# Kernel optimization log

Measured on AMD Instinct MI355X. Metric: run time of the kernel, lower is better.

## Reference

```python
import jax, jax.numpy as jnp
import numpy as np
import math

B, H, L, DK = 4, 16, 4096, 64
LK0 = 4096
LOG_LK = int(math.log(LK0))  # 8
LOG_L = int(math.log(L))     # 8
NC = 3
D_MODEL = H * DK             # 1024


def setup_inputs() -> dict:
    key = jax.random.key(0)
    ks = jax.random.split(key, 20)
    s = 0.02  # small init scale for stability of softmax/clustering
    f = jnp.float32
    return dict(
        Q=jax.random.normal(ks[0], (B, H, L, DK), f),
        K=jax.random.normal(ks[1], (B, H, LK0, DK), f),
        V=jax.random.normal(ks[2], (B, H, LK0, DK), f),
        shrink_k_w=jax.random.normal(ks[3], (LOG_LK, LK0), f) * s,
        shrink_k_b=jax.random.normal(ks[4], (LOG_LK,), f) * s,
        shrink_v_w=jax.random.normal(ks[5], (LOG_LK, LK0), f) * s,
        shrink_v_b=jax.random.normal(ks[6], (LOG_LK,), f) * s,
        shrink_q_w=jax.random.normal(ks[7], (LOG_L, L), f) * s,
        shrink_q_b=jax.random.normal(ks[8], (LOG_L,), f) * s,
        pk_w=jax.random.normal(ks[9], (NC, LOG_LK * D_MODEL), f) * s,
        pk_b=jax.random.normal(ks[10], (NC,), f) * s,
        pq_w=jax.random.normal(ks[11], (NC, LOG_L * D_MODEL), f) * s,
        pq_b=jax.random.normal(ks[12], (NC,), f) * s,
        qp_w=jax.random.normal(ks[13], (NC, NC), f) * s,
        qp_b=jax.random.normal(ks[14], (NC,), f) * s,
        kp_w=jax.random.normal(ks[15], (NC, NC), f) * s,
        kp_b=jax.random.normal(ks[16], (NC,), f) * s,
    )


def reference(Q, K, V, shrink_k_w, shrink_k_b, shrink_v_w, shrink_v_b,
              shrink_q_w, shrink_q_b, pk_w, pk_b, pq_w, pq_b,
              qp_w, qp_b, kp_w, kp_b):
    b, h, l, d_k = Q.shape
    # shrink along sequence axis (Linear over seq after permute in torch)
    Ks = jnp.einsum('bhkd,mk->bhmd', K, shrink_k_w) + shrink_k_b[None, None, :, None]
    Vs = jnp.einsum('bhkd,mk->bhmd', V, shrink_v_w) + shrink_v_b[None, None, :, None]
    Qs = jnp.einsum('bhqd,mq->bhmd', Q, shrink_q_w) + shrink_q_b[None, None, :, None]
    lk = Ks.shape[2]  # = LOG_LK
    # cluster logits -> soft assignments
    ckp = jax.nn.relu(Ks.reshape(b, -1) @ pk_w.T + pk_b)
    cqp = jax.nn.relu(Qs.reshape(b, -1) @ pq_w.T + pq_b)
    cluster_q = jax.nn.softmax(cqp @ qp_w.T + qp_b, axis=-1)
    cluster_k = jax.nn.softmax(ckp @ kp_w.T + kp_b, axis=-1)
    mu = jnp.mean(cluster_q, axis=0)
    sigma = jax.nn.softplus(jnp.std(cluster_k, axis=0, ddof=1))  # torch.std is unbiased
    logp = -0.5 * jnp.square((cluster_k - mu) / sigma) - jnp.log(sigma) - 0.5 * jnp.log(2.0 * jnp.pi)
    # CrossEntropyLoss with soft targets: -mean_b sum_c target*log_softmax(input)
    ce = jnp.mean(-jnp.sum(cluster_q * jax.nn.log_softmax(cluster_q, axis=-1), axis=-1))
    loss = -jnp.mean(logp) + ce

    inds_q = jnp.argmax(cluster_q, axis=-1)  # [b]
    inds_k = jnp.argmax(cluster_k, axis=-1)  # [b]
    # get_group masks whole batches whose cluster == i+1 (per-batch constant mask;
    # the reshape round-trip in the original is an identity on [b,h,seq,d])
    mask_tril = jnp.tril(jnp.ones((l, lk), dtype=bool))  # True positions get -1e9
    nc = qp_b.shape[0]
    scores_center = jnp.zeros((nc, b, h, l, lk), Q.dtype)
    row_idx = jnp.broadcast_to(inds_q[:, None, None], (b, h, l))  # q_ind[:,:,:,0]
    bi = jnp.arange(b)[:, None, None]
    hi = jnp.arange(h)[None, :, None]
    scale = 1.0 / jnp.sqrt(jnp.asarray(d_k, Q.dtype))
    for i in range(nc):
        gQ = jnp.where((inds_q != i + 1)[:, None, None, None], Q, 0.0)
        gK = jnp.where((inds_k != i + 1)[:, None, None, None], Ks, 0.0)
        s = jnp.einsum('bhqd,bhkd->bhqk', gQ, gK) * scale  # [b,h,l,lk]
        s = jnp.where(mask_tril, -1e9, s)
        # original repeats gK lk times along a c-axis, softmaxes, then means over c:
        # all c-copies are identical, so mean over c == the per-copy value; then [0]
        sm0 = jax.nn.softmax(s, axis=-1)[0]  # [h,l,lk] (batch 0, as in original)
        scores_center = scores_center.at[i, bi, hi, row_idx, :].set(
            jnp.broadcast_to(sm0, (b, h, l, lk)))
    final_score = jnp.max(scores_center, axis=0)  # [b,h,l,lk]
    attn = jax.nn.softmax(final_score, axis=-1)
    context = jnp.einsum('bhqk,bhkd->bhqd', attn, Vs)
    return context, loss
```

## Files before the change

kernel.cpp:

```cpp
#include <hip/hip_runtime.h>
#include <hip/hip_bf16.h>
#include <math.h>

#define BB   4
#define HH   16
#define LL   4096
#define DKK  64
#define MM   8
#define NCC  3
#define BH   (BB*HH)
#define ROWS_PER_CHUNK 512
#define NCHUNK (LL/ROWS_PER_CHUNK)
#define CTX_ELEMS (BB*HH*LL*DKK)

#define DOTS_OFF 98304

__global__ __launch_bounds__(256) void shrink_kernel(
    const float* __restrict__ Q, const float* __restrict__ K,
    const float* __restrict__ V,
    const float* __restrict__ skw, const float* __restrict__ svw,
    const float* __restrict__ sqw,
    float* __restrict__ ws)
{
    __shared__ float lds[12288];

    int bx    = blockIdx.x;
    int input = bx >> 9;
    int rem   = bx & 511;
    int bh    = rem >> 3;
    int chunk = rem & 7;

    const float* X; const float* W;
    if (input == 0)      { X = K; W = skw; }
    else if (input == 1) { X = V; W = svw; }
    else                 { X = Q; W = sqw; }

    int t  = threadIdx.x;
    int k0 = chunk * ROWS_PER_CHUNK;

    #pragma unroll
    for (int m = 0; m < MM; ++m)
        for (int k = t; k < ROWS_PER_CHUNK; k += 256)
            lds[k*8 + m] = W[m*LL + k0 + k];
    __syncthreads();

    int d4     = (t & 15) * 4;
    int stripe = t >> 4;

    const float* base = X + (size_t)bh * LL * DKK;

    float4 acc[MM];
    #pragma unroll
    for (int m = 0; m < MM; ++m) acc[m] = make_float4(0.f, 0.f, 0.f, 0.f);

    for (int i = 0; i < ROWS_PER_CHUNK/16; ++i) {
        int kp = i*16 + stripe;
        float4 v = *reinterpret_cast<const float4*>(
            base + (size_t)(k0 + kp) * DKK + d4);
        float4 w0 = *reinterpret_cast<const float4*>(&lds[kp*8]);
        float4 w1 = *reinterpret_cast<const float4*>(&lds[kp*8 + 4]);
        float wm[MM] = {w0.x, w0.y, w0.z, w0.w, w1.x, w1.y, w1.z, w1.w};
        #pragma unroll
        for (int m = 0; m < MM; ++m) {
            float w = wm[m];
            acc[m].x = fmaf(v.x, w, acc[m].x);
            acc[m].y = fmaf(v.y, w, acc[m].y);
            acc[m].z = fmaf(v.z, w, acc[m].z);
            acc[m].w = fmaf(v.w, w, acc[m].w);
        }
    }
    __syncthreads();

    float* red = lds + 4096;
    #pragma unroll
    for (int m = 0; m < MM; ++m) {
        red[t*32 + m*4 + 0] = acc[m].x;
        red[t*32 + m*4 + 1] = acc[m].y;
        red[t*32 + m*4 + 2] = acc[m].z;
        red[t*32 + m*4 + 3] = acc[m].w;
    }
    __syncthreads();

    float* wsb = ws + ((size_t)input * BH + bh) * 512;
    for (int out = t; out < 512; out += 256) {
        int m  = out >> 6;
        int d  = out & 63;
        int dg = d >> 2, dj = d & 3;
        float s = 0.f;
        #pragma unroll
        for (int st = 0; st < 16; ++st)
            s += red[(st*16 + dg)*32 + m*4 + dj];
        atomicAdd(wsb + out, s);
    }
}

__global__ __launch_bounds__(256) void dot_kernel(
    const float* __restrict__ ws,
    const float* __restrict__ skb, const float* __restrict__ sqb,
    const float* __restrict__ pk_w, const float* __restrict__ pk_b,
    const float* __restrict__ pq_w, const float* __restrict__ pq_b,
    float* __restrict__ dots)
{
    __shared__ float red[4];
    int idx = blockIdx.x;
    int isQ = idx >= 12;
    int g   = idx - (isQ ? 12 : 0);
    int b   = g / NCC;
    int c   = g % NCC;

    const float* xs   = ws + (size_t)(isQ ? 2 : 0) * (BH * 512) + (size_t)b * 8192;
    const float* pw   = (isQ ? pq_w : pk_w) + (size_t)c * 8192;
    const float* bias = isQ ? sqb : skb;

    float bl[MM];
    #pragma unroll
    for (int m = 0; m < MM; ++m) bl[m] = bias[m];

    int t = threadIdx.x;
    float acc = 0.f;
    #pragma unroll
    for (int i = 0; i < 8; ++i) {
        int e = i*256 + t;
        int m = (e >> 4) & 7;
        float4 x = *reinterpret_cast<const float4*>(xs + (size_t)e * 4);
        float4 w = *reinterpret_cast<const float4*>(pw + (size_t)e * 4);
        float bm = bl[m];
        acc = fmaf(x.x + bm, w.x, acc);
        acc = fmaf(x.y + bm, w.y, acc);
        acc = fmaf(x.z + bm, w.z, acc);
        acc = fmaf(x.w + bm, w.w, acc);
    }
    #pragma unroll
    for (int off = 1; off < 64; off <<= 1) acc += __shfl_xor(acc, off);
    int wave = t >> 6, lane = t & 63;
    if (lane == 0) red[wave] = acc;
    __syncthreads();
    if (t == 0) {
        float total = red[0] + red[1] + red[2] + red[3];
        float pb = (isQ ? pq_b : pk_b)[c];
        float r  = total + pb;
        dots[idx] = r > 0.f ? r : 0.f;
    }
}

__global__ __launch_bounds__(64) void final_kernel(
    const float* __restrict__ dots,
    const float* __restrict__ qp_w, const float* __restrict__ qp_b,
    const float* __restrict__ kp_w, const float* __restrict__ kp_b,
    float* __restrict__ out_loss)
{
    __shared__ float s_dots[24];
    __shared__ float s_qpw[9], s_qpb[3], s_kpw[9], s_kpb[3];
    int t = threadIdx.x;
    if (t < 24) s_dots[t] = dots[t];
    if (t < 9)  { s_qpw[t] = qp_w[t]; s_kpw[t] = kp_w[t]; }
    if (t < 3)  { s_qpb[t] = qp_b[t]; s_kpb[t] = kp_b[t]; }
    __syncthreads();

    if (t == 0) {
        float cq[BB][NCC], ck[BB][NCC];
        for (int b = 0; b < BB; ++b) {
            float lq[NCC], lk[NCC];
            for (int c = 0; c < NCC; ++c) {
                float sq = s_qpb[c], sk = s_kpb[c];
                for (int c2 = 0; c2 < NCC; ++c2) {
                    sq = fmaf(s_dots[12 + b*NCC + c2], s_qpw[c*NCC + c2], sq);
                    sk = fmaf(s_dots[b*NCC + c2],      s_kpw[c*NCC + c2], sk);
                }
                lq[c] = sq; lk[c] = sk;
            }
            float mq = fmaxf(fmaxf(lq[0], lq[1]), lq[2]);
            float mk = fmaxf(fmaxf(lk[0], lk[1]), lk[2]);
            float zq = 0.f, zk = 0.f;
            for (int c = 0; c < NCC; ++c) {
                cq[b][c] = expf(lq[c] - mq); zq += cq[b][c];
                ck[b][c] = expf(lk[c] - mk); zk += ck[b][c];
            }
            for (int c = 0; c < NCC; ++c) { cq[b][c] /= zq; ck[b][c] /= zk; }
        }
        float mu[NCC], mk_[NCC], sigma[NCC];
        for (int c = 0; c < NCC; ++c) {
            float s1 = 0.f, s2 = 0.f;
            for (int b = 0; b < BB; ++b) { s1 += cq[b][c]; s2 += ck[b][c]; }
            mu[c]  = s1 * 0.25f;
            mk_[c] = s2 * 0.25f;
        }
        for (int c = 0; c < NCC; ++c) {
            float v = 0.f;
            for (int b = 0; b < BB; ++b) {
                float d = ck[b][c] - mk_[c];
                v = fmaf(d, d, v);
            }
            float stdv = sqrtf(v / (BB - 1));
            sigma[c] = log1pf(expf(stdv));
        }
        const float HALF_LOG_2PI = 0.9189385332046727f;
        float sum_logp = 0.f;
        for (int b = 0; b < BB; ++b)
            for (int c = 0; c < NCC; ++c) {
                float z = (ck[b][c] - mu[c]) / sigma[c];
                sum_logp += -0.5f*z*z - logf(sigma[c]) - HALF_LOG_2PI;
            }
        float ce = 0.f;
        for (int b = 0; b < BB; ++b) {
            float mx = fmaxf(fmaxf(cq[b][0], cq[b][1]), cq[b][2]);
            float z = 0.f;
            for (int c = 0; c < NCC; ++c) z += expf(cq[b][c] - mx);
            float lse = mx + logf(z);
            float s = 0.f;
            for (int c = 0; c < NCC; ++c) s += cq[b][c] * (cq[b][c] - lse);
            ce += -s;
        }
        ce *= 0.25f;
        float loss = -(sum_logp / (BB * NCC)) + ce;
        out_loss[0] = loss;
    }
}

__global__ __launch_bounds__(256) void broadcast_kernel(
    const float* __restrict__ ws, const float* __restrict__ svb,
    float* __restrict__ out)
{
    int bx = blockIdx.x;
    int bh = bx >> 4;
    int lc = bx & 15;
    int t  = threadIdx.x;
    int d4     = (t & 15) * 4;
    int stripe = t >> 4;

    const float* vs = ws + ((size_t)1 * BH + bh) * 512;
    float bias = 0.f;
    #pragma unroll
    for (int m = 0; m < MM; ++m) bias += svb[m];
    bias *= 0.125f;

    float4 c = make_float4(bias, bias, bias, bias);
    #pragma unroll
    for (int m = 0; m < MM; ++m) {
        c.x += 0.125f * vs[m*64 + d4 + 0];
        c.y += 0.125f * vs[m*64 + d4 + 1];
        c.z += 0.125f * vs[m*64 + d4 + 2];
        c.w += 0.125f * vs[m*64 + d4 + 3];
    }

    float* obase = out + (size_t)bh * LL * DKK + (size_t)lc * 256 * DKK;
    #pragma unroll
    for (int i = 0; i < 16; ++i) {
        int l = i*16 + stripe;
        *reinterpret_cast<float4*>(obase + (size_t)l * DKK + d4) = c;
    }
}

extern "C" void kernel_launch(void* const* d_in, const int* in_sizes, int n_in,
                              void* d_out, int out_size, void* d_ws, size_t ws_size,
                              hipStream_t stream) {
    const float* Q    = (const float*)d_in[0];
    const float* K    = (const float*)d_in[1];
    const float* V    = (const float*)d_in[2];
    const float* skw  = (const float*)d_in[3];
    const float* skb  = (const float*)d_in[4];
    const float* svw  = (const float*)d_in[5];
    const float* svb  = (const float*)d_in[6];
    const float* sqw  = (const float*)d_in[7];
    const float* sqb  = (const float*)d_in[8];
    const float* pk_w = (const float*)d_in[9];
    const float* pk_b = (const float*)d_in[10];
    const float* pq_w = (const float*)d_in[11];
    const float* pq_b = (const float*)d_in[12];
    const float* qp_w = (const float*)d_in[13];
    const float* qp_b = (const float*)d_in[14];
    const float* kp_w = (const float*)d_in[15];
    const float* kp_b = (const float*)d_in[16];

    float* out = (float*)d_out;
    float* ws  = (float*)d_ws;

    hipMemsetAsync(ws, 0, (size_t)3 * BH * 512 * sizeof(float), stream);

    shrink_kernel<<<dim3(3 * BH * NCHUNK), dim3(256), 0, stream>>>(
        Q, K, V, skw, svw, sqw, ws);

    dot_kernel<<<dim3(24), dim3(256), 0, stream>>>(
        ws, skb, sqb, pk_w, pk_b, pq_w, pq_b, ws + DOTS_OFF);

    final_kernel<<<dim3(1), dim3(64), 0, stream>>>(
        ws + DOTS_OFF, qp_w, qp_b, kp_w, kp_b, out + (size_t)CTX_ELEMS);

    broadcast_kernel<<<dim3(BH * 16), dim3(256), 0, stream>>>(ws, svb, out);
}
```

Baseline: 276.8 us.

## Write per-chunk shrink partials without atomics and reduce them in consumers

The shrink kernel now uses 4 chunks of 1024 rows instead of 8 chunks of 512. It stores weights in m-major LDS, unrolls four row loads per iteration, and reduces across stripes with wave shuffles before a small padded LDS reduction. Each chunk writes its own partial slice, so the memset and global atomics go away, and the dot and broadcast kernels sum the four chunk partials when they read them. The cost is fewer blocks (768), which means less parallelism for the memory-bound streaming of Q, K and V, plus slightly more reads in the downstream kernels.

```diff
diff --git a/kernel.cpp b/kernel.cpp
--- a/kernel.cpp
+++ b/kernel.cpp
@@ -9,26 +9,27 @@
 #define MM   8
 #define NCC  3
 #define BH   (BB*HH)
-#define ROWS_PER_CHUNK 512
-#define NCHUNK (LL/ROWS_PER_CHUNK)
+#define NCHUNK 4
+#define ROWS_PER_CHUNK (LL/NCHUNK)
 #define CTX_ELEMS (BB*HH*LL*DKK)
 
-#define DOTS_OFF 98304
-
-__global__ __launch_bounds__(256) void shrink_kernel(
+#define DOTS_OFF (3*BH*NCHUNK*512)
+
+__global__ __launch_bounds__(256, 5) void shrink_kernel(
     const float* __restrict__ Q, const float* __restrict__ K,
     const float* __restrict__ V,
     const float* __restrict__ skw, const float* __restrict__ svw,
     const float* __restrict__ sqw,
     float* __restrict__ ws)
 {
-    __shared__ float lds[12288];
+    __shared__ float wlds[MM * ROWS_PER_CHUNK];
+    float* red = wlds;
 
     int bx    = blockIdx.x;
-    int input = bx >> 9;
-    int rem   = bx & 511;
-    int bh    = rem >> 3;
-    int chunk = rem & 7;
+    int input = bx >> 8;
+    int rem   = bx & 255;
+    int bh    = rem >> 2;
+    int chunk = rem & 3;
 
     const float* X; const float* W;
     if (input == 0)      { X = K; W = skw; }
@@ -40,57 +41,78 @@
 
     #pragma unroll
     for (int m = 0; m < MM; ++m)
-        for (int k = t; k < ROWS_PER_CHUNK; k += 256)
-            lds[k*8 + m] = W[m*LL + k0 + k];
-    __syncthreads();
-
-    int d4     = (t & 15) * 4;
+        #pragma unroll
+        for (int kk = 0; kk < ROWS_PER_CHUNK; kk += 256)
+            wlds[m*ROWS_PER_CHUNK + kk + t] = W[m*LL + k0 + kk + t];
+    __syncthreads();
+
+    int dg     = t & 15;
+    int d4     = dg * 4;
     int stripe = t >> 4;
 
-    const float* base = X + (size_t)bh * LL * DKK;
+    const float* base = X + (size_t)bh * LL * DKK + (size_t)k0 * DKK;
 
     float4 acc[MM];
     #pragma unroll
     for (int m = 0; m < MM; ++m) acc[m] = make_float4(0.f, 0.f, 0.f, 0.f);
 
-    for (int i = 0; i < ROWS_PER_CHUNK/16; ++i) {
-        int kp = i*16 + stripe;
-        float4 v = *reinterpret_cast<const float4*>(
-            base + (size_t)(k0 + kp) * DKK + d4);
-        float4 w0 = *reinterpret_cast<const float4*>(&lds[kp*8]);
-        float4 w1 = *reinterpret_cast<const float4*>(&lds[kp*8 + 4]);
-        float wm[MM] = {w0.x, w0.y, w0.z, w0.w, w1.x, w1.y, w1.z, w1.w};
+    for (int j = 0; j < ROWS_PER_CHUNK/64; ++j) {
+        float4 v[4];
+        #pragma unroll
+        for (int u = 0; u < 4; ++u) {
+            int row = j*64 + u*16 + stripe;
+            v[u] = *reinterpret_cast<const float4*>(base + (size_t)row * DKK + d4);
+        }
+        #pragma unroll
+        for (int u = 0; u < 4; ++u) {
+            int row = j*64 + u*16 + stripe;
+            #pragma unroll
+            for (int m = 0; m < MM; ++m) {
+                float w = wlds[m*ROWS_PER_CHUNK + row];
+                acc[m].x = fmaf(v[u].x, w, acc[m].x);
+                acc[m].y = fmaf(v[u].y, w, acc[m].y);
+                acc[m].z = fmaf(v[u].z, w, acc[m].z);
+                acc[m].w = fmaf(v[u].w, w, acc[m].w);
+            }
+        }
+    }
+
+    #pragma unroll
+    for (int m = 0; m < MM; ++m) {
+        acc[m].x += __shfl_xor(acc[m].x, 16);
+        acc[m].y += __shfl_xor(acc[m].y, 16);
+        acc[m].z += __shfl_xor(acc[m].z, 16);
+        acc[m].w += __shfl_xor(acc[m].w, 16);
+        acc[m].x += __shfl_xor(acc[m].x, 32);
+        acc[m].y += __shfl_xor(acc[m].y, 32);
+        acc[m].z += __shfl_xor(acc[m].z, 32);
+        acc[m].w += __shfl_xor(acc[m].w, 32);
+    }
+
+    __syncthreads();
+
+    int wave = t >> 6, lane = t & 63;
+    if (lane < 16) {
+        float* r = &red[(wave*16 + lane) * 33];
         #pragma unroll
         for (int m = 0; m < MM; ++m) {
-            float w = wm[m];
-            acc[m].x = fmaf(v.x, w, acc[m].x);
-            acc[m].y = fmaf(v.y, w, acc[m].y);
-            acc[m].z = fmaf(v.z, w, acc[m].z);
-            acc[m].w = fmaf(v.w, w, acc[m].w);
-        }
-    }
-    __syncthreads();
-
-    float* red = lds + 4096;
-    #pragma unroll
-    for (int m = 0; m < MM; ++m) {
-        red[t*32 + m*4 + 0] = acc[m].x;
-        red[t*32 + m*4 + 1] = acc[m].y;
-        red[t*32 + m*4 + 2] = acc[m].z;
-        red[t*32 + m*4 + 3] = acc[m].w;
-    }
-    __syncthreads();
-
-    float* wsb = ws + ((size_t)input * BH + bh) * 512;
-    for (int out = t; out < 512; out += 256) {
-        int m  = out >> 6;
-        int d  = out & 63;
-        int dg = d >> 2, dj = d & 3;
+            r[m*4 + 0] = acc[m].x;
+            r[m*4 + 1] = acc[m].y;
+            r[m*4 + 2] = acc[m].z;
+            r[m*4 + 3] = acc[m].w;
+        }
+    }
+    __syncthreads();
+
+    float* wsb = ws + (size_t)(((input*BH + bh)*NCHUNK + chunk)) * 512;
+    for (int o = t; o < 512; o += 256) {
+        int m = o >> 6, d = o & 63;
+        int dgg = d >> 2, dc = d & 3;
         float s = 0.f;
         #pragma unroll
-        for (int st = 0; st < 16; ++st)
-            s += red[(st*16 + dg)*32 + m*4 + dj];
-        atomicAdd(wsb + out, s);
+        for (int w = 0; w < 4; ++w)
+            s += red[(w*16 + dgg)*33 + m*4 + dc];
+        wsb[o] = s;
     }
 }
 
@@ -108,7 +130,7 @@
     int b   = g / NCC;
     int c   = g % NCC;
 
-    const float* xs   = ws + (size_t)(isQ ? 2 : 0) * (BH * 512) + (size_t)b * 8192;
+    int input = isQ ? 2 : 0;
     const float* pw   = (isQ ? pq_w : pk_w) + (size_t)c * 8192;
     const float* bias = isQ ? sqb : skb;
 
@@ -121,8 +143,16 @@
     #pragma unroll
     for (int i = 0; i < 8; ++i) {
         int e = i*256 + t;
+        int h = e >> 7;
         int m = (e >> 4) & 7;
-        float4 x = *reinterpret_cast<const float4*>(xs + (size_t)e * 4);
+        const float* xb = ws + (size_t)(((input*BH + b*HH + h)*NCHUNK)) * 512
+                             + (size_t)(e & 127) * 4;
+        float4 x = make_float4(0.f, 0.f, 0.f, 0.f);
+        #pragma unroll
+        for (int ch = 0; ch < NCHUNK; ++ch) {
+            float4 p = *reinterpret_cast<const float4*>(xb + ch*512);
+            x.x += p.x; x.y += p.y; x.z += p.z; x.w += p.w;
+        }
         float4 w = *reinterpret_cast<const float4*>(pw + (size_t)e * 4);
         float bm = bl[m];
         acc = fmaf(x.x + bm, w.x, acc);
@@ -228,7 +258,7 @@
     int d4     = (t & 15) * 4;
     int stripe = t >> 4;
 
-    const float* vs = ws + ((size_t)1 * BH + bh) * 512;
+    const float* vsb = ws + (size_t)((1*BH + bh)*NCHUNK) * 512;
     float bias = 0.f;
     #pragma unroll
     for (int m = 0; m < MM; ++m) bias += svb[m];
@@ -237,10 +267,14 @@
     float4 c = make_float4(bias, bias, bias, bias);
     #pragma unroll
     for (int m = 0; m < MM; ++m) {
-        c.x += 0.125f * vs[m*64 + d4 + 0];
-        c.y += 0.125f * vs[m*64 + d4 + 1];
-        c.z += 0.125f * vs[m*64 + d4 + 2];
-        c.w += 0.125f * vs[m*64 + d4 + 3];
+        #pragma unroll
+        for (int ch = 0; ch < NCHUNK; ++ch) {
+            const float* p = vsb + ch*512 + m*64 + d4;
+            c.x += 0.125f * p[0];
+            c.y += 0.125f * p[1];
+            c.z += 0.125f * p[2];
+            c.w += 0.125f * p[3];
+        }
     }
 
     float* obase = out + (size_t)bh * LL * DKK + (size_t)lc * 256 * DKK;
@@ -275,7 +309,6 @@
     float* out = (float*)d_out;
     float* ws  = (float*)d_ws;
 
-    hipMemsetAsync(ws, 0, (size_t)3 * BH * 512 * sizeof(float), stream);
 
     shrink_kernel<<<dim3(3 * BH * NCHUNK), dim3(256), 0, stream>>>(
         Q, K, V, skw, svw, sqw, ws);
```

New measurement: 263.0 us. 1.05x faster.
